# Performance work log

Measured on AMD Instinct MI355X. Metric: run time of the kernel, lower is better.

The kernel has to match this reference:

```python
import jax, jax.numpy as jnp
import numpy as np

N = 100000
DEG = 16
E = N * DEG
IN_F = 128
OUT_F = 64
ALPHA = 0.2  # LeakyReLU negative slope


def setup_inputs() -> dict:
    key = jax.random.key(0)
    k1, k2, k3, k4, k5, k6 = jax.random.split(key, 6)
    x = jax.random.normal(k1, (N, IN_F), dtype=jnp.float32)
    # src = repeat(arange(N), DEG) guarantees every node has outgoing edges
    # (original torch code divides by the out-edge score sum -> NaN otherwise).
    src = jnp.repeat(jnp.arange(N, dtype=jnp.int64), DEG)
    dst = jax.random.randint(k2, (E,), 0, N, dtype=jnp.int64)
    edges = jnp.stack([src, dst], axis=0)
    # Conv1d(in, out, k=1, bias=False) == linear with weight [out, in]
    w_seq = jax.random.normal(k3, (OUT_F, IN_F), dtype=jnp.float32) / np.sqrt(IN_F)
    # a_1, a_2: Conv1d(out, 1, k=1) with bias
    a1_w = jax.random.normal(k4, (OUT_F,), dtype=jnp.float32) / np.sqrt(OUT_F)
    a1_b = jnp.zeros((), dtype=jnp.float32)
    a2_w = jax.random.normal(k5, (OUT_F,), dtype=jnp.float32) / np.sqrt(OUT_F)
    a2_b = jnp.zeros((), dtype=jnp.float32)
    bias = jnp.zeros((OUT_F,), dtype=jnp.float32)
    return {"x": x, "edges": edges, "w_seq": w_seq, "a1_w": a1_w,
            "a1_b": a1_b, "a2_w": a2_w, "a2_b": a2_b, "bias": bias}


def reference(x, edges, w_seq, a1_w, a1_b, a2_w, a2_b, bias):
    src, dst = edges[0], edges[1]
    feat = x @ w_seq.T                       # [N, OUT_F]
    a1 = feat @ a1_w + a1_b                  # [N]
    a2 = feat @ a2_w + a2_b                  # [N]
    score = a1[src] + a2[dst]                # [E]
    score = jnp.exp(jax.nn.leaky_relu(score, ALPHA))
    score_sum = jax.ops.segment_sum(score, src, num_segments=N)  # [N]
    # sparse COO (score at (src,dst)) @ feat == segment_sum of score * feat[dst]
    msgs = score[:, None] * feat[dst]        # [E, OUT_F]
    agg = jax.ops.segment_sum(msgs, src, num_segments=N)         # [N, OUT_F]
    out = agg / score_sum[:, None] + bias
    return out
```

## Files before the change

### kernel.cpp

```cpp
#include <hip/hip_runtime.h>
#include <hip/hip_bf16.h>
#include <stdint.h>

#define N_NODES 100000
#define DEG 16
#define IN_F 128
#define OUT_F 64
#define ALPHA 0.2f

typedef __attribute__((ext_vector_type(8))) short short8;
typedef __attribute__((ext_vector_type(4))) float f32x4;
typedef __attribute__((ext_vector_type(4))) int i32x4;
typedef __attribute__((ext_vector_type(4))) unsigned int u32x4;
typedef __attribute__((ext_vector_type(2))) unsigned int u32x2;

static __device__ __forceinline__ unsigned int pack2bf(float lo, float hi) {
    __hip_bfloat162 h = __float22bfloat162_rn(make_float2(lo, hi));
    unsigned int u; __builtin_memcpy(&u, &h, 4); return u;
}
static __device__ __forceinline__ unsigned short f2bf(float f) {
    __hip_bfloat16 h = __float2bfloat16(f);
    unsigned short u; __builtin_memcpy(&u, &h, 2); return u;
}

__global__ __launch_bounds__(256) void prep_kernel(
    const float* __restrict__ w, const float* __restrict__ a1w,
    unsigned short* __restrict__ wb, float* __restrict__ v1)
{
    int idx = blockIdx.x * 256 + threadIdx.x;
    if (idx < OUT_F * IN_F) wb[idx] = f2bf(w[idx]);
    if (blockIdx.x == 0 && threadIdx.x < IN_F) {
        int k = threadIdx.x;
        float acc = 0.f;
        #pragma unroll
        for (int f = 0; f < OUT_F; ++f) acc += w[f * IN_F + k] * a1w[f];
        v1[k] = acc;
    }
}

__global__ __launch_bounds__(64) void gat_feat_kernel(
    const float* __restrict__ x, const unsigned short* __restrict__ wb,
    const float* __restrict__ v1, const float* __restrict__ a1bp,
    unsigned short* __restrict__ featb, float* __restrict__ a1)
{
    __shared__ __align__(16) unsigned short lds[32][64];
    const int lane = threadIdx.x & 63;
    const int r = lane & 15;
    const int g = lane >> 4;
    const unsigned base = blockIdx.x * 32;

    f32x4 xr[2][4][2];
    #pragma unroll
    for (int mt = 0; mt < 2; ++mt) {
        const float* xrow = x + (size_t)(base + mt * 16 + r) * IN_F + g * 8;
        #pragma unroll
        for (int ks = 0; ks < 4; ++ks) {
            xr[mt][ks][0] = __builtin_nontemporal_load((const f32x4*)(xrow + ks * 32));
            xr[mt][ks][1] = __builtin_nontemporal_load((const f32x4*)(xrow + ks * 32 + 4));
        }
    }

    f32x4 acc[2][4];
    #pragma unroll
    for (int mt = 0; mt < 2; ++mt)
        #pragma unroll
        for (int ft = 0; ft < 4; ++ft) acc[mt][ft] = (f32x4){0.f, 0.f, 0.f, 0.f};
    float p1[2] = {0.f, 0.f};

    #pragma unroll
    for (int ks = 0; ks < 4; ++ks) {
        short8 bf[4];
        #pragma unroll
        for (int ft = 0; ft < 4; ++ft)
            bf[ft] = *(const short8*)(wb + (ft * 16 + r) * IN_F + ks * 32 + g * 8);
        const float* vp1 = v1 + ks * 32 + g * 8;
        f32x4 v10 = *(const f32x4*)(vp1), v11 = *(const f32x4*)(vp1 + 4);
        #pragma unroll
        for (int mt = 0; mt < 2; ++mt) {
            f32x4 x0 = xr[mt][ks][0], x1 = xr[mt][ks][1];
            #pragma unroll
            for (int j = 0; j < 4; ++j)
                p1[mt] += x0[j] * v10[j] + x1[j] * v11[j];
            u32x4 au;
            au[0] = pack2bf(x0[0], x0[1]);
            au[1] = pack2bf(x0[2], x0[3]);
            au[2] = pack2bf(x1[0], x1[1]);
            au[3] = pack2bf(x1[2], x1[3]);
            short8 af; __builtin_memcpy(&af, &au, 16);
            #pragma unroll
            for (int ft = 0; ft < 4; ++ft)
                acc[mt][ft] = __builtin_amdgcn_mfma_f32_16x16x32_bf16(af, bf[ft], acc[mt][ft], 0, 0, 0);
        }
    }

    #pragma unroll
    for (int mt = 0; mt < 2; ++mt) {
        p1[mt] += __shfl_xor(p1[mt], 16, 64);
        p1[mt] += __shfl_xor(p1[mt], 32, 64);
    }
    if (lane < 16) {
        float b1 = a1bp[0];
        #pragma unroll
        for (int mt = 0; mt < 2; ++mt)
            a1[base + mt * 16 + lane] = p1[mt] + b1;
    }

    #pragma unroll
    for (int mt = 0; mt < 2; ++mt)
        #pragma unroll
        for (int ft = 0; ft < 4; ++ft) {
            const int cp = (ft * 16 + r) ^ (g << 4);
            #pragma unroll
            for (int reg = 0; reg < 4; ++reg)
                lds[mt * 16 + g * 4 + reg][cp] = f2bf(acc[mt][ft][reg]);
        }
    char* gdst = (char*)featb + (size_t)base * (OUT_F * 2);
    #pragma unroll
    for (int t = 0; t < 4; ++t) {
        const int row = t * 8 + (lane >> 3);
        const int cl  = (lane & 7) * 8;
        const int cp  = cl ^ (((row >> 2) & 3) << 4);
        i32x4 v = *(const i32x4*)(&lds[row][cp]);
        *(i32x4*)(gdst + (size_t)row * 128 + cl * 2) = v;
    }
}

#define BFLO(w_) __uint_as_float((w_) << 16)
#define BFHI(w_) __uint_as_float((w_) & 0xffff0000u)

__global__ __launch_bounds__(256) void gat_agg_kernel(
    const int* __restrict__ dst, const unsigned short* __restrict__ featb,
    const float* __restrict__ a1, const float* __restrict__ a2w,
    const float* __restrict__ a2bp, const float* __restrict__ bias,
    float* __restrict__ out)
{
    const int wid  = threadIdx.x >> 6;
    const int lane = threadIdx.x & 63;
    const int e0 = lane & 15;
    const int sb = lane & 48;
    const int i = (blockIdx.x * 4 + wid) * 4 + (lane >> 4);

    const int d = dst[i * DEG + e0];

#define GATH(t) \
    const int de##t = __shfl(d, sb + (t), 64); \
    const u32x2 u##t = *(const u32x2*)(featb + (unsigned)de##t * OUT_F + e0 * 4);
    GATH(0)  GATH(1)  GATH(2)  GATH(3)
    GATH(4)  GATH(5)  GATH(6)  GATH(7)
    GATH(8)  GATH(9)  GATH(10) GATH(11)
    GATH(12) GATH(13) GATH(14) GATH(15)
#undef GATH

    const float a1i = a1[i] + a2bp[0];
    const f32x4 aw = *(const f32x4*)(a2w + e0 * 4);
    const f32x4 bv = *(const f32x4*)(bias + e0 * 4);

    float acc0 = 0.f, acc1 = 0.f, acc2 = 0.f, acc3 = 0.f, ssum = 0.f;
#define EDGE(t) { \
    const float f0 = BFLO(u##t[0]), f1 = BFHI(u##t[0]); \
    const float f2 = BFLO(u##t[1]), f3 = BFHI(u##t[1]); \
    float p = f0 * aw[0] + f1 * aw[1] + f2 * aw[2] + f3 * aw[3]; \
    p += __shfl_xor(p, 1, 64); p += __shfl_xor(p, 2, 64); \
    p += __shfl_xor(p, 4, 64); p += __shfl_xor(p, 8, 64); \
    const float z = a1i + p; \
    const float s = __expf(fmaxf(z, ALPHA * z)); \
    ssum += s; \
    acc0 += s * f0; acc1 += s * f1; acc2 += s * f2; acc3 += s * f3; }
    EDGE(0)  EDGE(1)  EDGE(2)  EDGE(3)
    EDGE(4)  EDGE(5)  EDGE(6)  EDGE(7)
    EDGE(8)  EDGE(9)  EDGE(10) EDGE(11)
    EDGE(12) EDGE(13) EDGE(14) EDGE(15)
#undef EDGE

    const float inv = 1.0f / ssum;
    f32x4 o;
    o[0] = acc0 * inv + bv[0];
    o[1] = acc1 * inv + bv[1];
    o[2] = acc2 * inv + bv[2];
    o[3] = acc3 * inv + bv[3];
    __builtin_nontemporal_store(o, (f32x4*)(out + (unsigned)i * OUT_F + e0 * 4));
}

extern "C" void kernel_launch(void* const* d_in, const int* in_sizes, int n_in,
                              void* d_out, int out_size, void* d_ws, size_t ws_size,
                              hipStream_t stream) {
    (void)in_sizes; (void)n_in; (void)out_size; (void)ws_size;
    const float* x    = (const float*)d_in[0];
    const int*   edges= (const int*)d_in[1];
    const float* w    = (const float*)d_in[2];
    const float* a1w  = (const float*)d_in[3];
    const float* a1b  = (const float*)d_in[4];
    const float* a2w  = (const float*)d_in[5];
    const float* a2b  = (const float*)d_in[6];
    const float* bias = (const float*)d_in[7];
    float* out = (float*)d_out;

    unsigned short* featb = (unsigned short*)d_ws;
    float* a1 = (float*)((char*)d_ws + (size_t)N_NODES * OUT_F * 2);
    float* v1 = a1 + N_NODES;
    unsigned short* wb = (unsigned short*)(v1 + IN_F);

    const int* dst = edges + (size_t)N_NODES * DEG;

    prep_kernel<<<dim3((OUT_F * IN_F + 255) / 256), dim3(256), 0, stream>>>(
        w, a1w, wb, v1);
    gat_feat_kernel<<<dim3(N_NODES / 32), dim3(64), 0, stream>>>(
        x, wb, v1, a1b, featb, a1);
    gat_agg_kernel<<<dim3(N_NODES / 16), dim3(256), 0, stream>>>(
        dst, featb, a1, a2w, a2b, bias, out);
}
```

Measured before the change: 65.65 us.

## Compute a1 from MFMA accumulators and use 4-wave feat blocks

The precomputed v1 = W^T·a1_w vector and the per-lane fp32 dot products on x are removed. a1 is now computed from the fp32 MFMA accumulators times a1_w, followed by a 16-lane shuffle reduction. The feature kernel moves from one wave per block to four independent waves per block with per-wave LDS tiles, and all W fragments are hoisted into registers up front. The LDS XOR swizzle and nontemporal x loads are dropped, which may bring back LDS bank conflicts on the transposing writes and raises register pressure.

```diff
diff --git a/kernel.cpp b/kernel.cpp
--- a/kernel.cpp
+++ b/kernel.cpp
@@ -24,63 +24,46 @@
 }
 
 __global__ __launch_bounds__(256) void prep_kernel(
-    const float* __restrict__ w, const float* __restrict__ a1w,
-    unsigned short* __restrict__ wb, float* __restrict__ v1)
+    const float* __restrict__ w, unsigned short* __restrict__ wb)
 {
     int idx = blockIdx.x * 256 + threadIdx.x;
     if (idx < OUT_F * IN_F) wb[idx] = f2bf(w[idx]);
-    if (blockIdx.x == 0 && threadIdx.x < IN_F) {
-        int k = threadIdx.x;
-        float acc = 0.f;
-        #pragma unroll
-        for (int f = 0; f < OUT_F; ++f) acc += w[f * IN_F + k] * a1w[f];
-        v1[k] = acc;
-    }
-}
-
-__global__ __launch_bounds__(64) void gat_feat_kernel(
+}
+
+__global__ __launch_bounds__(256) void gat_feat_kernel(
     const float* __restrict__ x, const unsigned short* __restrict__ wb,
-    const float* __restrict__ v1, const float* __restrict__ a1bp,
+    const float* __restrict__ a1w, const float* __restrict__ a1bp,
     unsigned short* __restrict__ featb, float* __restrict__ a1)
 {
-    __shared__ __align__(16) unsigned short lds[32][64];
+    __shared__ __align__(16) unsigned short lds[4][32][64];
+    const int wid  = threadIdx.x >> 6;
     const int lane = threadIdx.x & 63;
     const int r = lane & 15;
     const int g = lane >> 4;
-    const unsigned base = blockIdx.x * 32;
-
-    f32x4 xr[2][4][2];
+    const int base = (blockIdx.x * 4 + wid) * 32;
+    if (base >= N_NODES) return;
+
+    short8 bfrag[4][4];
+    #pragma unroll
+    for (int ft = 0; ft < 4; ++ft)
+        #pragma unroll
+        for (int ks = 0; ks < 4; ++ks)
+            bfrag[ft][ks] = *(const short8*)(wb + (ft * 16 + r) * IN_F + ks * 32 + g * 8);
+
+    f32x4 acc[2][4];
+    #pragma unroll
+    for (int mt = 0; mt < 2; ++mt)
+        #pragma unroll
+        for (int ft = 0; ft < 4; ++ft) acc[mt][ft] = (f32x4){0.f, 0.f, 0.f, 0.f};
+
     #pragma unroll
     for (int mt = 0; mt < 2; ++mt) {
-        const float* xrow = x + (size_t)(base + mt * 16 + r) * IN_F + g * 8;
+        const float* xrow = x + (size_t)(base + mt * 16 + r) * IN_F;
         #pragma unroll
         for (int ks = 0; ks < 4; ++ks) {
-            xr[mt][ks][0] = __builtin_nontemporal_load((const f32x4*)(xrow + ks * 32));
-            xr[mt][ks][1] = __builtin_nontemporal_load((const f32x4*)(xrow + ks * 32 + 4));
-        }
-    }
-
-    f32x4 acc[2][4];
-    #pragma unroll
-    for (int mt = 0; mt < 2; ++mt)
-        #pragma unroll
-        for (int ft = 0; ft < 4; ++ft) acc[mt][ft] = (f32x4){0.f, 0.f, 0.f, 0.f};
-    float p1[2] = {0.f, 0.f};
-
-    #pragma unroll
-    for (int ks = 0; ks < 4; ++ks) {
-        short8 bf[4];
-        #pragma unroll
-        for (int ft = 0; ft < 4; ++ft)
-            bf[ft] = *(const short8*)(wb + (ft * 16 + r) * IN_F + ks * 32 + g * 8);
-        const float* vp1 = v1 + ks * 32 + g * 8;
-        f32x4 v10 = *(const f32x4*)(vp1), v11 = *(const f32x4*)(vp1 + 4);
-        #pragma unroll
-        for (int mt = 0; mt < 2; ++mt) {
-            f32x4 x0 = xr[mt][ks][0], x1 = xr[mt][ks][1];
-            #pragma unroll
-            for (int j = 0; j < 4; ++j)
-                p1[mt] += x0[j] * v10[j] + x1[j] * v11[j];
+            const float* xp = xrow + ks * 32 + g * 8;
+            f32x4 x0 = *(const f32x4*)(xp);
+            f32x4 x1 = *(const f32x4*)(xp + 4);
             u32x4 au;
             au[0] = pack2bf(x0[0], x0[1]);
             au[1] = pack2bf(x0[2], x0[3]);
@@ -89,39 +72,50 @@
             short8 af; __builtin_memcpy(&af, &au, 16);
             #pragma unroll
             for (int ft = 0; ft < 4; ++ft)
-                acc[mt][ft] = __builtin_amdgcn_mfma_f32_16x16x32_bf16(af, bf[ft], acc[mt][ft], 0, 0, 0);
+                acc[mt][ft] = __builtin_amdgcn_mfma_f32_16x16x32_bf16(af, bfrag[ft][ks], acc[mt][ft], 0, 0, 0);
         }
     }
 
-    #pragma unroll
-    for (int mt = 0; mt < 2; ++mt) {
-        p1[mt] += __shfl_xor(p1[mt], 16, 64);
-        p1[mt] += __shfl_xor(p1[mt], 32, 64);
+    float w1v[4];
+    #pragma unroll
+    for (int ft = 0; ft < 4; ++ft) w1v[ft] = a1w[ft * 16 + r];
+    float p1[2][4] = {{0.f,0.f,0.f,0.f},{0.f,0.f,0.f,0.f}};
+    #pragma unroll
+    for (int mt = 0; mt < 2; ++mt)
+        #pragma unroll
+        for (int ft = 0; ft < 4; ++ft)
+            #pragma unroll
+            for (int reg = 0; reg < 4; ++reg)
+                p1[mt][reg] += acc[mt][ft][reg] * w1v[ft];
+    #pragma unroll
+    for (int m = 1; m <= 8; m <<= 1)
+        #pragma unroll
+        for (int mt = 0; mt < 2; ++mt)
+            #pragma unroll
+            for (int reg = 0; reg < 4; ++reg)
+                p1[mt][reg] += __shfl_xor(p1[mt][reg], m, 64);
+    if (r == 0) {
+        float b1 = a1bp[0];
+        #pragma unroll
+        for (int mt = 0; mt < 2; ++mt)
+            #pragma unroll
+            for (int reg = 0; reg < 4; ++reg)
+                a1[base + mt * 16 + g * 4 + reg] = p1[mt][reg] + b1;
     }
-    if (lane < 16) {
-        float b1 = a1bp[0];
-        #pragma unroll
-        for (int mt = 0; mt < 2; ++mt)
-            a1[base + mt * 16 + lane] = p1[mt] + b1;
-    }
 
     #pragma unroll
     for (int mt = 0; mt < 2; ++mt)
         #pragma unroll
-        for (int ft = 0; ft < 4; ++ft) {
-            const int cp = (ft * 16 + r) ^ (g << 4);
-            #pragma unroll
-            for (int reg = 0; reg < 4; ++reg)
-                lds[mt * 16 + g * 4 + reg][cp] = f2bf(acc[mt][ft][reg]);
-        }
+        for (int ft = 0; ft < 4; ++ft)
+            #pragma unroll
+            for (int reg = 0; reg < 4; ++reg)
+                lds[wid][mt * 16 + g * 4 + reg][ft * 16 + r] = f2bf(acc[mt][ft][reg]);
+    const char* lsrc = (const char*)(&lds[wid][0][0]);
     char* gdst = (char*)featb + (size_t)base * (OUT_F * 2);
     #pragma unroll
     for (int t = 0; t < 4; ++t) {
-        const int row = t * 8 + (lane >> 3);
-        const int cl  = (lane & 7) * 8;
-        const int cp  = cl ^ (((row >> 2) & 3) << 4);
-        i32x4 v = *(const i32x4*)(&lds[row][cp]);
-        *(i32x4*)(gdst + (size_t)row * 128 + cl * 2) = v;
+        i32x4 v = *(const i32x4*)(lsrc + t * 1024 + lane * 16);
+        *(i32x4*)(gdst + t * 1024 + lane * 16) = v;
     }
 }
 
@@ -197,15 +191,13 @@
 
     unsigned short* featb = (unsigned short*)d_ws;
     float* a1 = (float*)((char*)d_ws + (size_t)N_NODES * OUT_F * 2);
-    float* v1 = a1 + N_NODES;
-    unsigned short* wb = (unsigned short*)(v1 + IN_F);
+    unsigned short* wb = (unsigned short*)(a1 + N_NODES);
 
     const int* dst = edges + (size_t)N_NODES * DEG;
 
-    prep_kernel<<<dim3((OUT_F * IN_F + 255) / 256), dim3(256), 0, stream>>>(
-        w, a1w, wb, v1);
-    gat_feat_kernel<<<dim3(N_NODES / 32), dim3(64), 0, stream>>>(
-        x, wb, v1, a1b, featb, a1);
+    prep_kernel<<<dim3((OUT_F * IN_F + 255) / 256), dim3(256), 0, stream>>>(w, wb);
+    gat_feat_kernel<<<dim3((N_NODES + 127) / 128), dim3(256), 0, stream>>>(
+        x, wb, a1w, a1b, featb, a1);
     gat_agg_kernel<<<dim3(N_NODES / 16), dim3(256), 0, stream>>>(
         dst, featb, a1, a2w, a2b, bias, out);
 }
```

After: 60.14 us. 8.4% less time.
